# Performance work log

Hardware: AMD Instinct MI355X
Metric: run time of the kernel (lower is better)

The kernel has to match this reference:

```python
import jax, jax.numpy as jnp
import numpy as np

EPS = 1e-07
ONEHOT_MIN = 1e-4  # clamp floor applied to the one-hot labels


def setup_inputs() -> dict:
    key = jax.random.key(0)
    k1, k2 = jax.random.split(key)
    pred = jax.random.normal(k1, (4096, 50001), dtype=jnp.float32)
    labels = jax.random.randint(k2, (4096,), 0, 50000, dtype=jnp.int64)
    return {"pred": pred, "labels": labels}


def reference(pred, labels):
    # Drop the last logit column, as in the torch module.
    logits = pred[..., :-1]  # [N, 50000]
    logp = jax.nn.log_softmax(logits, axis=1)
    # Standard CE (mean reduction), gathered at the true label.
    logp_true = jnp.take_along_axis(logp, labels[:, None], axis=1)[:, 0]
    ce = -jnp.mean(logp_true)
    # Reverse CE. clamp(one_hot, 1e-4, 1.0) has log(1)=0 at the true class and
    # log(1e-4) everywhere else, so sum_j p_j*log(onehot_clamped_j)
    # = log(1e-4) * (sum_j p_j - p_true) exactly -- no [N, V] one-hot needed.
    p = jnp.clip(jnp.exp(logp), EPS, 1.0)  # clamp(softmax, eps, 1.0)
    p_true = jnp.take_along_axis(p, labels[:, None], axis=1)[:, 0]
    log_low = jnp.log(jnp.asarray(ONEHOT_MIN, dtype=p.dtype))
    rce = -(log_low * (jnp.sum(p, axis=1) - p_true))  # [N]
    a = jnp.asarray(1.0, dtype=p.dtype)
    b = jnp.asarray(1.0, dtype=p.dtype)
    return a * ce + b * jnp.mean(rce)
```

## Files before the change

### kernel.cpp

```cpp
#include <hip/hip_runtime.h>
#include <cstdint>
#include <cstddef>

#define ROWS   4096
#define COLS   50000
#define STRIDE 50001
#define NTHR   256

typedef float f4 __attribute__((ext_vector_type(4)));

__device__ const float NEG_LOG_LOW = 9.210340371976184f;

__global__ __launch_bounds__(NTHR) void sce_row_kernel(
        const float* __restrict__ pred,
        const int* __restrict__ labels,
        float* __restrict__ row_loss)
{
    const int row = blockIdx.x;
    const int tid = threadIdx.x;
    const float* rowp = pred + (size_t)row * STRIDE;

    __shared__ float s_xtrue;
    __shared__ float s_part[NTHR / 64];
    if (tid == 0) {
        int l = labels[row];
        s_xtrue = rowp[l];
    }

    const uintptr_t a = (uintptr_t)rowp;
    const int mis  = (int)((a & 15) >> 2);
    const int lead = (4 - mis) & 3;
    const int nrem = COLS - lead;
    const int nvec = nrem >> 2;
    const int tail = nrem & 3;
    const f4* __restrict__ v4 = (const f4*)(rowp + lead);

    float sum0 = 0.0f, sum1 = 0.0f;
    int i = tid;
    for (; i + NTHR < nvec; i += 2 * NTHR) {
        f4 va = __builtin_nontemporal_load(v4 + i);
        f4 vb = __builtin_nontemporal_load(v4 + i + NTHR);
        sum0 += __expf(va.x) + __expf(va.y) + __expf(va.z) + __expf(va.w);
        sum1 += __expf(vb.x) + __expf(vb.y) + __expf(vb.z) + __expf(vb.w);
    }
    if (i < nvec) {
        f4 va = __builtin_nontemporal_load(v4 + i);
        sum0 += __expf(va.x) + __expf(va.y) + __expf(va.z) + __expf(va.w);
    }
    float sum = sum0 + sum1;

    if (tid < lead)
        sum += __expf(rowp[tid]);
    if (tid >= 64 && tid < 64 + tail)
        sum += __expf(rowp[lead + 4 * nvec + (tid - 64)]);

    #pragma unroll
    for (int off = 32; off > 0; off >>= 1)
        sum += __shfl_down(sum, off, 64);
    if ((tid & 63) == 0) s_part[tid >> 6] = sum;
    __syncthreads();

    if (tid == 0) {
        float s = s_part[0] + s_part[1] + s_part[2] + s_part[3];
        float logZ   = logf(s);
        float xt     = s_xtrue;
        float p_true = __expf(xt) / s;
        row_loss[row] = (logZ - xt) + NEG_LOG_LOW * (1.0f - p_true);
    }
}

__global__ __launch_bounds__(NTHR) void sce_reduce_kernel(
        const float* __restrict__ row_loss,
        float* __restrict__ out)
{
    const int tid = threadIdx.x;
    double sum = 0.0;
    for (int i = tid; i < ROWS; i += NTHR)
        sum += (double)row_loss[i];
    #pragma unroll
    for (int off = 32; off > 0; off >>= 1)
        sum += __shfl_down(sum, off, 64);
    __shared__ double s_part[NTHR / 64];
    if ((tid & 63) == 0) s_part[tid >> 6] = sum;
    __syncthreads();
    if (tid == 0)
        out[0] = (float)((s_part[0] + s_part[1] + s_part[2] + s_part[3]) *
                         (1.0 / (double)ROWS));
}

extern "C" void kernel_launch(void* const* d_in, const int* in_sizes, int n_in,
                              void* d_out, int out_size, void* d_ws, size_t ws_size,
                              hipStream_t stream)
{
    const float* pred   = (const float*)d_in[0];
    const int*   labels = (const int*)d_in[1];
    float*       out    = (float*)d_out;
    float*       rl     = (float*)d_ws;

    sce_row_kernel<<<ROWS, NTHR, 0, stream>>>(pred, labels, rl);
    sce_reduce_kernel<<<1, NTHR, 0, stream>>>(rl, out);
}
```

Baseline: 136.8 us.

## Fuse final mean into row kernel via fixed-point atomics and unroll loads 4x

Drops the separate single-block reduction kernel. Each row block now atomically adds its loss, scaled to 64-bit fixed point, into a workspace counter, and the last block to finish writes the mean. A memset of the workspace is added before the launch. The main load loop is also unrolled from 2 to 4 vector loads per thread to raise memory-level parallelism. This trades one kernel launch for a memset plus per-row atomics, and the fixed-point conversion assumes row losses are non-negative and small enough to fit the scale.

```diff
diff --git a/kernel.cpp b/kernel.cpp
--- a/kernel.cpp
+++ b/kernel.cpp
@@ -10,11 +10,13 @@
 typedef float f4 __attribute__((ext_vector_type(4)));
 
 __device__ const float NEG_LOG_LOW = 9.210340371976184f;
+#define FIXED_SCALE 4294967296.0
 
 __global__ __launch_bounds__(NTHR) void sce_row_kernel(
         const float* __restrict__ pred,
         const int* __restrict__ labels,
-        float* __restrict__ row_loss)
+        float* __restrict__ out,
+        unsigned long long* __restrict__ ws)
 {
     const int row = blockIdx.x;
     const int tid = threadIdx.x;
@@ -35,19 +37,23 @@
     const int tail = nrem & 3;
     const f4* __restrict__ v4 = (const f4*)(rowp + lead);
 
-    float sum0 = 0.0f, sum1 = 0.0f;
+    float sum0 = 0.0f, sum1 = 0.0f, sum2 = 0.0f, sum3 = 0.0f;
     int i = tid;
-    for (; i + NTHR < nvec; i += 2 * NTHR) {
+    for (; i + 3 * NTHR < nvec; i += 4 * NTHR) {
         f4 va = __builtin_nontemporal_load(v4 + i);
         f4 vb = __builtin_nontemporal_load(v4 + i + NTHR);
+        f4 vc = __builtin_nontemporal_load(v4 + i + 2 * NTHR);
+        f4 vd = __builtin_nontemporal_load(v4 + i + 3 * NTHR);
         sum0 += __expf(va.x) + __expf(va.y) + __expf(va.z) + __expf(va.w);
         sum1 += __expf(vb.x) + __expf(vb.y) + __expf(vb.z) + __expf(vb.w);
+        sum2 += __expf(vc.x) + __expf(vc.y) + __expf(vc.z) + __expf(vc.w);
+        sum3 += __expf(vd.x) + __expf(vd.y) + __expf(vd.z) + __expf(vd.w);
     }
-    if (i < nvec) {
+    for (; i < nvec; i += NTHR) {
         f4 va = __builtin_nontemporal_load(v4 + i);
         sum0 += __expf(va.x) + __expf(va.y) + __expf(va.z) + __expf(va.w);
     }
-    float sum = sum0 + sum1;
+    float sum = (sum0 + sum1) + (sum2 + sum3);
 
     if (tid < lead)
         sum += __expf(rowp[tid]);
@@ -65,27 +71,18 @@
         float logZ   = logf(s);
         float xt     = s_xtrue;
         float p_true = __expf(xt) / s;
-        row_loss[row] = (logZ - xt) + NEG_LOG_LOW * (1.0f - p_true);
+        float row_loss = (logZ - xt) + NEG_LOG_LOW * (1.0f - p_true);
+
+        unsigned long long fx =
+            (unsigned long long)((double)row_loss * FIXED_SCALE);
+        atomicAdd(ws, fx);
+        __threadfence();
+        unsigned int old = atomicAdd((unsigned int*)(ws + 1), 1u);
+        if (old == ROWS - 1) {
+            unsigned long long total = atomicAdd(ws, 0ULL);
+            out[0] = (float)((double)total * (1.0 / FIXED_SCALE / (double)ROWS));
+        }
     }
-}
-
-__global__ __launch_bounds__(NTHR) void sce_reduce_kernel(
-        const float* __restrict__ row_loss,
-        float* __restrict__ out)
-{
-    const int tid = threadIdx.x;
-    double sum = 0.0;
-    for (int i = tid; i < ROWS; i += NTHR)
-        sum += (double)row_loss[i];
-    #pragma unroll
-    for (int off = 32; off > 0; off >>= 1)
-        sum += __shfl_down(sum, off, 64);
-    __shared__ double s_part[NTHR / 64];
-    if ((tid & 63) == 0) s_part[tid >> 6] = sum;
-    __syncthreads();
-    if (tid == 0)
-        out[0] = (float)((s_part[0] + s_part[1] + s_part[2] + s_part[3]) *
-                         (1.0 / (double)ROWS));
 }
 
 extern "C" void kernel_launch(void* const* d_in, const int* in_sizes, int n_in,
@@ -95,8 +92,8 @@
     const float* pred   = (const float*)d_in[0];
     const int*   labels = (const int*)d_in[1];
     float*       out    = (float*)d_out;
-    float*       rl     = (float*)d_ws;
+    unsigned long long* ws = (unsigned long long*)d_ws;
 
-    sce_row_kernel<<<ROWS, NTHR, 0, stream>>>(pred, labels, rl);
-    sce_reduce_kernel<<<1, NTHR, 0, stream>>>(rl, out);
+    hipMemsetAsync(d_ws, 0, 16, stream);
+    sce_row_kernel<<<ROWS, NTHR, 0, stream>>>(pred, labels, out, ws);
 }
```

Measured after the change: 342.3 us. 150% more time.
